# Performance work log

Hardware: AMD Instinct MI355X
Metric: run time of the kernel (lower is better)

Reference implementation:

```python
import jax, jax.numpy as jnp
import numpy as np

SAMPLE_THRESH = 0.05  # self.sample_thresh


def grid_sample_bilinear_zeros(img, pts):
    """torch.nn.functional.grid_sample with mode='bilinear', align_corners=False,
    padding_mode='zeros'. img: [C, H, W]; pts: [N, 2] with (x, y) in [-1, 1].
    Returns [C, N]."""
    C, H, W = img.shape
    # align_corners=False unnormalization
    x = (pts[:, 0] + 1.0) * (W / 2.0) - 0.5
    y = (pts[:, 1] + 1.0) * (H / 2.0) - 0.5
    x0 = jnp.floor(x)
    y0 = jnp.floor(y)
    wx1 = x - x0
    wy1 = y - y0
    wx0 = 1.0 - wx1
    wy0 = 1.0 - wy1

    def gather(xi, yi):
        valid = (xi >= 0) & (xi < W) & (yi >= 0) & (yi < H)
        xi_c = jnp.clip(xi, 0, W - 1).astype(jnp.int32)
        yi_c = jnp.clip(yi, 0, H - 1).astype(jnp.int32)
        v = img[:, yi_c, xi_c]  # [C, N]
        return v * valid.astype(img.dtype)[None, :]

    out = (gather(x0, y0) * (wx0 * wy0)[None, :]
           + gather(x0 + 1, y0) * (wx1 * wy0)[None, :]
           + gather(x0, y0 + 1) * (wx0 * wy1)[None, :]
           + gather(x0 + 1, y0 + 1) * (wx1 * wy1)[None, :])
    return out


def setup_inputs() -> dict:
    key = jax.random.key(0)
    k1, k2, k3, k4 = jax.random.split(key, 4)
    N_A, N_B = 8192, 8192
    H, W2 = 504, 1008  # warp is [hs, 2*ws, 4] per post_process
    x_A = jax.random.uniform(k1, (N_A, 2), jnp.float32, -1.0, 1.0)
    x_B = jax.random.uniform(k2, (N_B, 2), jnp.float32, -1.0, 1.0)
    warp = jax.random.uniform(k3, (H, W2, 4), jnp.float32, -1.0, 1.0)
    certainty = jax.random.uniform(k4, (H, W2), jnp.float32, 0.0, 1.0)
    return {"x_A": x_A, "x_B": x_B, "warp": warp, "certainty": certainty}


def reference(x_A, x_B, warp, certainty):
    # --- match_keypoints ---
    # x_A_to_B = grid_sample(warp[..., -2:].permute(2,0,1)[None], x_A[None,None])[0,:,0].mT
    flow_img = jnp.transpose(warp[..., -2:], (2, 0, 1))  # [2, H, 2W]
    x_A_to_B = grid_sample_bilinear_zeros(flow_img, x_A).T  # [N_A, 2]
    cert_A_to_B = grid_sample_bilinear_zeros(certainty[None], x_A)[0]  # [N_A]

    # D = torch.cdist(x_A_to_B, x_B) via |a|^2 + |b|^2 - 2 a.b
    a2 = jnp.sum(x_A_to_B * x_A_to_B, axis=-1)  # [N_A]
    b2 = jnp.sum(x_B * x_B, axis=-1)            # [N_B]
    D2 = a2[:, None] + b2[None, :] - 2.0 * (x_A_to_B @ x_B.T)
    D = jnp.sqrt(jnp.maximum(D2, 1e-12))  # [N_A, N_B]

    # mutual nearest-neighbor mask with certainty threshold
    row_min = jnp.min(D, axis=-1, keepdims=True)
    col_min = jnp.min(D, axis=-2, keepdims=True)
    mask = (D == row_min) & (D == col_min) & (cert_A_to_B[:, None] > SAMPLE_THRESH)

    # jit-compatible equivalent of torch.nonzero: distances at mutual-NN pairs,
    # zero elsewhere. nonzero entries == matched (inds_A, inds_B) pairs.
    return jnp.where(mask, D, 0.0)
```

## Files before the change

kernel.cpp:

```cpp
#include <hip/hip_runtime.h>
#include <math.h>

#define SAMPLE_THRESH 0.05f

__device__ __forceinline__ float dist_exact(float xa0, float xa1, float a2,
                                            float xb0, float xb1, float b2) {
    float p  = __fmul_rn(xa1, xb1);
    float q  = __fmaf_rn(xa0, xb0, p);
    float s  = __fadd_rn(a2, b2);
    float d2 = __fmaf_rn(-2.0f, q, s);
    d2 = fmaxf(d2, 1e-12f);
    return __fsqrt_rn(d2);
}

__global__ __launch_bounds__(256) void sample_kernel(
    const float* __restrict__ xA, const float* __restrict__ xB,
    const float4* __restrict__ warp, const float* __restrict__ cert,
    float4* __restrict__ Apack, float* __restrict__ b2arr,
    int nA, int nB, int H, int W) {
    int i = blockIdx.x * blockDim.x + threadIdx.x;
    if (i < nA) {
        float px = xA[2 * i + 0], py = xA[2 * i + 1];
        float xf = (px + 1.0f) * (0.5f * (float)W) - 0.5f;
        float yf = (py + 1.0f) * (0.5f * (float)H) - 0.5f;
        float x0f = floorf(xf), y0f = floorf(yf);
        float wx1 = xf - x0f, wy1 = yf - y0f;
        float wx0 = 1.0f - wx1, wy0 = 1.0f - wy1;
        int x0 = (int)x0f, y0 = (int)y0f;
        float fx = 0.0f, fy = 0.0f, cv = 0.0f;
#pragma unroll
        for (int dy = 0; dy < 2; ++dy) {
#pragma unroll
            for (int dx = 0; dx < 2; ++dx) {
                int xi = x0 + dx, yi = y0 + dy;
                float vm = (xi >= 0 && xi < W && yi >= 0 && yi < H) ? 1.0f : 0.0f;
                int xc = min(max(xi, 0), W - 1);
                int yc = min(max(yi, 0), H - 1);
                int idx = yc * W + xc;
                float4 wv = warp[idx];
                float  c  = cert[idx];
                float wgt = (dx ? wx1 : wx0) * (dy ? wy1 : wy0);
                fx += (wv.z * vm) * wgt;
                fy += (wv.w * vm) * wgt;
                cv += (c    * vm) * wgt;
            }
        }
        float a2 = fx * fx + fy * fy;
        Apack[i] = make_float4(fx, fy, a2, cv);
    }
    if (i < nB) {
        float b0 = xB[2 * i + 0], b1 = xB[2 * i + 1];
        b2arr[i] = b0 * b0 + b1 * b1;
    }
}

__global__ __launch_bounds__(256) void rowmin_kernel(
    const float4* __restrict__ Apack, const float2* __restrict__ xB,
    const float* __restrict__ b2arr, float4* __restrict__ rowpack,
    int nA, int nB) {
    int wave = (int)((blockIdx.x * blockDim.x + threadIdx.x) >> 6);
    int lane = threadIdx.x & 63;
    int i0 = wave * 4;
    if (i0 >= nA) return;
    float4 A0 = Apack[i0 + 0], A1 = Apack[i0 + 1];
    float4 A2 = Apack[i0 + 2], A3 = Apack[i0 + 3];
    float m0 = 1e30f, m1 = 1e30f, m2 = 1e30f, m3 = 1e30f;
    for (int j = lane; j < nB; j += 64) {
        float2 b = xB[j];
        float bb = b2arr[j];
        m0 = fminf(m0, dist_exact(A0.x, A0.y, A0.z, b.x, b.y, bb));
        m1 = fminf(m1, dist_exact(A1.x, A1.y, A1.z, b.x, b.y, bb));
        m2 = fminf(m2, dist_exact(A2.x, A2.y, A2.z, b.x, b.y, bb));
        m3 = fminf(m3, dist_exact(A3.x, A3.y, A3.z, b.x, b.y, bb));
    }
#pragma unroll
    for (int o = 32; o; o >>= 1) {
        m0 = fminf(m0, __shfl_xor(m0, o, 64));
        m1 = fminf(m1, __shfl_xor(m1, o, 64));
        m2 = fminf(m2, __shfl_xor(m2, o, 64));
        m3 = fminf(m3, __shfl_xor(m3, o, 64));
    }
    if (lane == 0) {
        rowpack[i0 + 0] = make_float4(A0.x, A0.y, A0.z, (A0.w > SAMPLE_THRESH) ? m0 : -1.0f);
        rowpack[i0 + 1] = make_float4(A1.x, A1.y, A1.z, (A1.w > SAMPLE_THRESH) ? m1 : -1.0f);
        rowpack[i0 + 2] = make_float4(A2.x, A2.y, A2.z, (A2.w > SAMPLE_THRESH) ? m2 : -1.0f);
        rowpack[i0 + 3] = make_float4(A3.x, A3.y, A3.z, (A3.w > SAMPLE_THRESH) ? m3 : -1.0f);
    }
}

__global__ __launch_bounds__(256) void colmin_kernel(
    const float4* __restrict__ Apack, const float2* __restrict__ xB,
    const float* __restrict__ b2arr, float4* __restrict__ colpack,
    int nA, int nB) {
    int wave = (int)((blockIdx.x * blockDim.x + threadIdx.x) >> 6);
    int lane = threadIdx.x & 63;
    int j0 = wave * 4;
    if (j0 >= nB) return;
    float2 b0 = xB[j0 + 0], b1 = xB[j0 + 1], b2v = xB[j0 + 2], b3 = xB[j0 + 3];
    float bb0 = b2arr[j0 + 0], bb1 = b2arr[j0 + 1], bb2 = b2arr[j0 + 2], bb3 = b2arr[j0 + 3];
    float m0 = 1e30f, m1 = 1e30f, m2 = 1e30f, m3 = 1e30f;
    for (int i = lane; i < nA; i += 64) {
        float4 a = Apack[i];
        m0 = fminf(m0, dist_exact(a.x, a.y, a.z, b0.x, b0.y, bb0));
        m1 = fminf(m1, dist_exact(a.x, a.y, a.z, b1.x, b1.y, bb1));
        m2 = fminf(m2, dist_exact(a.x, a.y, a.z, b2v.x, b2v.y, bb2));
        m3 = fminf(m3, dist_exact(a.x, a.y, a.z, b3.x, b3.y, bb3));
    }
#pragma unroll
    for (int o = 32; o; o >>= 1) {
        m0 = fminf(m0, __shfl_xor(m0, o, 64));
        m1 = fminf(m1, __shfl_xor(m1, o, 64));
        m2 = fminf(m2, __shfl_xor(m2, o, 64));
        m3 = fminf(m3, __shfl_xor(m3, o, 64));
    }
    if (lane == 0) {
        colpack[j0 + 0] = make_float4(b0.x, b0.y, bb0, m0);
        colpack[j0 + 1] = make_float4(b1.x, b1.y, bb1, m1);
        colpack[j0 + 2] = make_float4(b2v.x, b2v.y, bb2, m2);
        colpack[j0 + 3] = make_float4(b3.x, b3.y, bb3, m3);
    }
}

#define TI 64
#define TJ 1024
__global__ __launch_bounds__(256) void out_kernel(
    const float4* __restrict__ rowpack, const float4* __restrict__ colpack,
    float* __restrict__ out, int N) {
    __shared__ float4 cp[TJ];
    __shared__ float4 rp[TI];
    int tid = threadIdx.x;
    int j0 = blockIdx.x * TJ;
    int i0 = blockIdx.y * TI;
    for (int k = tid; k < TJ; k += 256) cp[k] = colpack[j0 + k];
    if (tid < TI) rp[tid] = rowpack[i0 + tid];
    __syncthreads();
    float4 c0 = cp[tid * 4 + 0], c1 = cp[tid * 4 + 1];
    float4 c2 = cp[tid * 4 + 2], c3 = cp[tid * 4 + 3];
    size_t base = (size_t)i0 * (size_t)N + (size_t)j0 + (size_t)tid * 4;
    for (int r = 0; r < TI; ++r) {
        float4 a = rp[r];
        float d0 = dist_exact(a.x, a.y, a.z, c0.x, c0.y, c0.z);
        float d1 = dist_exact(a.x, a.y, a.z, c1.x, c1.y, c1.z);
        float d2 = dist_exact(a.x, a.y, a.z, c2.x, c2.y, c2.z);
        float d3 = dist_exact(a.x, a.y, a.z, c3.x, c3.y, c3.z);
        float4 o;
        o.x = (d0 == a.w && d0 == c0.w) ? d0 : 0.0f;
        o.y = (d1 == a.w && d1 == c1.w) ? d1 : 0.0f;
        o.z = (d2 == a.w && d2 == c2.w) ? d2 : 0.0f;
        o.w = (d3 == a.w && d3 == c3.w) ? d3 : 0.0f;
        *(float4*)(out + base + (size_t)r * (size_t)N) = o;
    }
}

extern "C" void kernel_launch(void* const* d_in, const int* in_sizes, int n_in,
                              void* d_out, int out_size, void* d_ws, size_t ws_size,
                              hipStream_t stream) {
    const float* xA   = (const float*)d_in[0];
    const float* xB   = (const float*)d_in[1];
    const float* warp = (const float*)d_in[2];
    const float* cert = (const float*)d_in[3];
    int nA = in_sizes[0] / 2;
    int nB = in_sizes[1] / 2;
    const int H = 504, W = 1008;
    float* out = (float*)d_out;

    char* ws = (char*)d_ws;
    size_t oA   = 0;
    size_t oB2  = oA + (size_t)nA * sizeof(float4);
    size_t oRow = (oB2 + (size_t)nB * sizeof(float) + 15) & ~(size_t)15;
    size_t oCol = oRow + (size_t)nA * sizeof(float4);
    float4* Apack   = (float4*)(ws + oA);
    float*  b2arr   = (float*)(ws + oB2);
    float4* rowpack = (float4*)(ws + oRow);
    float4* colpack = (float4*)(ws + oCol);

    int nmax = nA > nB ? nA : nB;
    sample_kernel<<<(nmax + 255) / 256, 256, 0, stream>>>(
        xA, xB, (const float4*)warp, cert, Apack, b2arr, nA, nB, H, W);

    int rowWaves = nA / 4;
    rowmin_kernel<<<(rowWaves * 64 + 255) / 256, 256, 0, stream>>>(
        Apack, (const float2*)xB, b2arr, rowpack, nA, nB);

    int colWaves = nB / 4;
    colmin_kernel<<<(colWaves * 64 + 255) / 256, 256, 0, stream>>>(
        Apack, (const float2*)xB, b2arr, colpack, nA, nB);

    dim3 grid(nB / TJ, nA / TI);
    out_kernel<<<grid, 256, 0, stream>>>(rowpack, colpack, out, nB);
}
```

Measured before the change: 372.2 us.

## Merge row/col min kernels and defer sqrt to after min reduction

Fuses the row-min and column-min passes into one launch, with waves split between the two roles so both run concurrently. It also reduces over squared distances and takes the sqrt only once per row or column minimum, instead of once per pair. B points are packed as float4 (x, y, |b|^2) so each needs one vector load. This cuts per-pair sqrt cost and one launch; since sqrt and the clamp are monotonic, min(sqrt(clamp(d2))) equals sqrt(clamp(min(d2))), so the equality tests in the output kernel stay exact.

```diff
diff --git a/kernel.cpp b/kernel.cpp
--- a/kernel.cpp
+++ b/kernel.cpp
@@ -3,20 +3,22 @@
 
 #define SAMPLE_THRESH 0.05f
 
-__device__ __forceinline__ float dist_exact(float xa0, float xa1, float a2,
-                                            float xb0, float xb1, float b2) {
+__device__ __forceinline__ float d2_exact(float xa0, float xa1, float a2,
+                                          float xb0, float xb1, float b2) {
     float p  = __fmul_rn(xa1, xb1);
     float q  = __fmaf_rn(xa0, xb0, p);
     float s  = __fadd_rn(a2, b2);
-    float d2 = __fmaf_rn(-2.0f, q, s);
-    d2 = fmaxf(d2, 1e-12f);
-    return __fsqrt_rn(d2);
+    return __fmaf_rn(-2.0f, q, s);
+}
+
+__device__ __forceinline__ float D_from_d2(float d2) {
+    return __fsqrt_rn(fmaxf(d2, 1e-12f));
 }
 
 __global__ __launch_bounds__(256) void sample_kernel(
     const float* __restrict__ xA, const float* __restrict__ xB,
     const float4* __restrict__ warp, const float* __restrict__ cert,
-    float4* __restrict__ Apack, float* __restrict__ b2arr,
+    float4* __restrict__ Apack, float4* __restrict__ Bpack,
     int nA, int nB, int H, int W) {
     int i = blockIdx.x * blockDim.x + threadIdx.x;
     if (i < nA) {
@@ -50,74 +52,67 @@
     }
     if (i < nB) {
         float b0 = xB[2 * i + 0], b1 = xB[2 * i + 1];
-        b2arr[i] = b0 * b0 + b1 * b1;
+        Bpack[i] = make_float4(b0, b1, b0 * b0 + b1 * b1, 0.0f);
     }
 }
 
-__global__ __launch_bounds__(256) void rowmin_kernel(
-    const float4* __restrict__ Apack, const float2* __restrict__ xB,
-    const float* __restrict__ b2arr, float4* __restrict__ rowpack,
+__global__ __launch_bounds__(256) void min_kernel(
+    const float4* __restrict__ Apack, const float4* __restrict__ Bpack,
+    float4* __restrict__ rowpack, float4* __restrict__ colpack,
     int nA, int nB) {
-    int wave = (int)((blockIdx.x * blockDim.x + threadIdx.x) >> 6);
+    int gwave = (int)((blockIdx.x * blockDim.x + threadIdx.x) >> 6);
     int lane = threadIdx.x & 63;
-    int i0 = wave * 4;
-    if (i0 >= nA) return;
-    float4 A0 = Apack[i0 + 0], A1 = Apack[i0 + 1];
-    float4 A2 = Apack[i0 + 2], A3 = Apack[i0 + 3];
+    int nRowWaves = nA / 4;
     float m0 = 1e30f, m1 = 1e30f, m2 = 1e30f, m3 = 1e30f;
-    for (int j = lane; j < nB; j += 64) {
-        float2 b = xB[j];
-        float bb = b2arr[j];
-        m0 = fminf(m0, dist_exact(A0.x, A0.y, A0.z, b.x, b.y, bb));
-        m1 = fminf(m1, dist_exact(A1.x, A1.y, A1.z, b.x, b.y, bb));
-        m2 = fminf(m2, dist_exact(A2.x, A2.y, A2.z, b.x, b.y, bb));
-        m3 = fminf(m3, dist_exact(A3.x, A3.y, A3.z, b.x, b.y, bb));
-    }
+    if (gwave < nRowWaves) {
+        int i0 = gwave * 4;
+        float4 A0 = Apack[i0 + 0], A1 = Apack[i0 + 1];
+        float4 A2 = Apack[i0 + 2], A3 = Apack[i0 + 3];
+        for (int j = lane; j < nB; j += 64) {
+            float4 b = Bpack[j];
+            m0 = fminf(m0, d2_exact(A0.x, A0.y, A0.z, b.x, b.y, b.z));
+            m1 = fminf(m1, d2_exact(A1.x, A1.y, A1.z, b.x, b.y, b.z));
+            m2 = fminf(m2, d2_exact(A2.x, A2.y, A2.z, b.x, b.y, b.z));
+            m3 = fminf(m3, d2_exact(A3.x, A3.y, A3.z, b.x, b.y, b.z));
+        }
 #pragma unroll
-    for (int o = 32; o; o >>= 1) {
-        m0 = fminf(m0, __shfl_xor(m0, o, 64));
-        m1 = fminf(m1, __shfl_xor(m1, o, 64));
-        m2 = fminf(m2, __shfl_xor(m2, o, 64));
-        m3 = fminf(m3, __shfl_xor(m3, o, 64));
-    }
-    if (lane == 0) {
-        rowpack[i0 + 0] = make_float4(A0.x, A0.y, A0.z, (A0.w > SAMPLE_THRESH) ? m0 : -1.0f);
-        rowpack[i0 + 1] = make_float4(A1.x, A1.y, A1.z, (A1.w > SAMPLE_THRESH) ? m1 : -1.0f);
-        rowpack[i0 + 2] = make_float4(A2.x, A2.y, A2.z, (A2.w > SAMPLE_THRESH) ? m2 : -1.0f);
-        rowpack[i0 + 3] = make_float4(A3.x, A3.y, A3.z, (A3.w > SAMPLE_THRESH) ? m3 : -1.0f);
-    }
-}
-
-__global__ __launch_bounds__(256) void colmin_kernel(
-    const float4* __restrict__ Apack, const float2* __restrict__ xB,
-    const float* __restrict__ b2arr, float4* __restrict__ colpack,
-    int nA, int nB) {
-    int wave = (int)((blockIdx.x * blockDim.x + threadIdx.x) >> 6);
-    int lane = threadIdx.x & 63;
-    int j0 = wave * 4;
-    if (j0 >= nB) return;
-    float2 b0 = xB[j0 + 0], b1 = xB[j0 + 1], b2v = xB[j0 + 2], b3 = xB[j0 + 3];
-    float bb0 = b2arr[j0 + 0], bb1 = b2arr[j0 + 1], bb2 = b2arr[j0 + 2], bb3 = b2arr[j0 + 3];
-    float m0 = 1e30f, m1 = 1e30f, m2 = 1e30f, m3 = 1e30f;
-    for (int i = lane; i < nA; i += 64) {
-        float4 a = Apack[i];
-        m0 = fminf(m0, dist_exact(a.x, a.y, a.z, b0.x, b0.y, bb0));
-        m1 = fminf(m1, dist_exact(a.x, a.y, a.z, b1.x, b1.y, bb1));
-        m2 = fminf(m2, dist_exact(a.x, a.y, a.z, b2v.x, b2v.y, bb2));
-        m3 = fminf(m3, dist_exact(a.x, a.y, a.z, b3.x, b3.y, bb3));
-    }
+        for (int o = 32; o; o >>= 1) {
+            m0 = fminf(m0, __shfl_xor(m0, o, 64));
+            m1 = fminf(m1, __shfl_xor(m1, o, 64));
+            m2 = fminf(m2, __shfl_xor(m2, o, 64));
+            m3 = fminf(m3, __shfl_xor(m3, o, 64));
+        }
+        if (lane == 0) {
+            rowpack[i0 + 0] = make_float4(A0.x, A0.y, A0.z, (A0.w > SAMPLE_THRESH) ? D_from_d2(m0) : -1.0f);
+            rowpack[i0 + 1] = make_float4(A1.x, A1.y, A1.z, (A1.w > SAMPLE_THRESH) ? D_from_d2(m1) : -1.0f);
+            rowpack[i0 + 2] = make_float4(A2.x, A2.y, A2.z, (A2.w > SAMPLE_THRESH) ? D_from_d2(m2) : -1.0f);
+            rowpack[i0 + 3] = make_float4(A3.x, A3.y, A3.z, (A3.w > SAMPLE_THRESH) ? D_from_d2(m3) : -1.0f);
+        }
+    } else {
+        int j0 = (gwave - nRowWaves) * 4;
+        if (j0 >= nB) return;
+        float4 B0 = Bpack[j0 + 0], B1 = Bpack[j0 + 1];
+        float4 B2 = Bpack[j0 + 2], B3 = Bpack[j0 + 3];
+        for (int i = lane; i < nA; i += 64) {
+            float4 a = Apack[i];
+            m0 = fminf(m0, d2_exact(a.x, a.y, a.z, B0.x, B0.y, B0.z));
+            m1 = fminf(m1, d2_exact(a.x, a.y, a.z, B1.x, B1.y, B1.z));
+            m2 = fminf(m2, d2_exact(a.x, a.y, a.z, B2.x, B2.y, B2.z));
+            m3 = fminf(m3, d2_exact(a.x, a.y, a.z, B3.x, B3.y, B3.z));
+        }
 #pragma unroll
-    for (int o = 32; o; o >>= 1) {
-        m0 = fminf(m0, __shfl_xor(m0, o, 64));
-        m1 = fminf(m1, __shfl_xor(m1, o, 64));
-        m2 = fminf(m2, __shfl_xor(m2, o, 64));
-        m3 = fminf(m3, __shfl_xor(m3, o, 64));
-    }
-    if (lane == 0) {
-        colpack[j0 + 0] = make_float4(b0.x, b0.y, bb0, m0);
-        colpack[j0 + 1] = make_float4(b1.x, b1.y, bb1, m1);
-        colpack[j0 + 2] = make_float4(b2v.x, b2v.y, bb2, m2);
-        colpack[j0 + 3] = make_float4(b3.x, b3.y, bb3, m3);
+        for (int o = 32; o; o >>= 1) {
+            m0 = fminf(m0, __shfl_xor(m0, o, 64));
+            m1 = fminf(m1, __shfl_xor(m1, o, 64));
+            m2 = fminf(m2, __shfl_xor(m2, o, 64));
+            m3 = fminf(m3, __shfl_xor(m3, o, 64));
+        }
+        if (lane == 0) {
+            colpack[j0 + 0] = make_float4(B0.x, B0.y, B0.z, D_from_d2(m0));
+            colpack[j0 + 1] = make_float4(B1.x, B1.y, B1.z, D_from_d2(m1));
+            colpack[j0 + 2] = make_float4(B2.x, B2.y, B2.z, D_from_d2(m2));
+            colpack[j0 + 3] = make_float4(B3.x, B3.y, B3.z, D_from_d2(m3));
+        }
     }
 }
 
@@ -139,10 +134,10 @@
     size_t base = (size_t)i0 * (size_t)N + (size_t)j0 + (size_t)tid * 4;
     for (int r = 0; r < TI; ++r) {
         float4 a = rp[r];
-        float d0 = dist_exact(a.x, a.y, a.z, c0.x, c0.y, c0.z);
-        float d1 = dist_exact(a.x, a.y, a.z, c1.x, c1.y, c1.z);
-        float d2 = dist_exact(a.x, a.y, a.z, c2.x, c2.y, c2.z);
-        float d3 = dist_exact(a.x, a.y, a.z, c3.x, c3.y, c3.z);
+        float d0 = D_from_d2(d2_exact(a.x, a.y, a.z, c0.x, c0.y, c0.z));
+        float d1 = D_from_d2(d2_exact(a.x, a.y, a.z, c1.x, c1.y, c1.z));
+        float d2 = D_from_d2(d2_exact(a.x, a.y, a.z, c2.x, c2.y, c2.z));
+        float d3 = D_from_d2(d2_exact(a.x, a.y, a.z, c3.x, c3.y, c3.z));
         float4 o;
         o.x = (d0 == a.w && d0 == c0.w) ? d0 : 0.0f;
         o.y = (d1 == a.w && d1 == c1.w) ? d1 : 0.0f;
@@ -165,26 +160,18 @@
     float* out = (float*)d_out;
 
     char* ws = (char*)d_ws;
-    size_t oA   = 0;
-    size_t oB2  = oA + (size_t)nA * sizeof(float4);
-    size_t oRow = (oB2 + (size_t)nB * sizeof(float) + 15) & ~(size_t)15;
-    size_t oCol = oRow + (size_t)nA * sizeof(float4);
-    float4* Apack   = (float4*)(ws + oA);
-    float*  b2arr   = (float*)(ws + oB2);
-    float4* rowpack = (float4*)(ws + oRow);
-    float4* colpack = (float4*)(ws + oCol);
+    float4* Apack   = (float4*)ws;
+    float4* Bpack   = Apack + nA;
+    float4* rowpack = Bpack + nB;
+    float4* colpack = rowpack + nA;
 
     int nmax = nA > nB ? nA : nB;
     sample_kernel<<<(nmax + 255) / 256, 256, 0, stream>>>(
-        xA, xB, (const float4*)warp, cert, Apack, b2arr, nA, nB, H, W);
+        xA, xB, (const float4*)warp, cert, Apack, Bpack, nA, nB, H, W);
 
-    int rowWaves = nA / 4;
-    rowmin_kernel<<<(rowWaves * 64 + 255) / 256, 256, 0, stream>>>(
-        Apack, (const float2*)xB, b2arr, rowpack, nA, nB);
-
-    int colWaves = nB / 4;
-    colmin_kernel<<<(colWaves * 64 + 255) / 256, 256, 0, stream>>>(
-        Apack, (const float2*)xB, b2arr, colpack, nA, nB);
+    int totWaves = nA / 4 + nB / 4;
+    min_kernel<<<(totWaves * 64 + 255) / 256, 256, 0, stream>>>(
+        Apack, Bpack, rowpack, colpack, nA, nB);
 
     dim3 grid(nB / TJ, nA / TI);
     out_kernel<<<grid, 256, 0, stream>>>(rowpack, colpack, out, nB);
```

Result: faster. 325.3 us (-12.6%).
